# Optimization experiments

Hardware: AMD Instinct MI355X
Metric: run time of the kernel (lower is better)

## Reference

```python
import jax, jax.numpy as jnp
import numpy as np

H_STEP = 0.1
DT_MOMENTUM = 1.0
NUM_STEPS = 5
PAD_IDX = 0


def setup_inputs() -> dict:
    key = jax.random.key(0)
    k0, k1, k2, k3 = jax.random.split(key, 4)
    V, D, S, H, B = 32000, 512, 1024, 2048, 32
    table = jax.random.normal(k0, (V, D), jnp.float32) * 0.02
    log_masses = jnp.zeros((S,), jnp.float32)
    W1 = jax.random.normal(k1, (H, D), jnp.float32) * (1.0 / np.sqrt(D))
    b1 = jnp.zeros((H,), jnp.float32)
    W2 = jax.random.normal(k2, (1, H), jnp.float32) * (1.0 / np.sqrt(H))
    b2 = jnp.zeros((1,), jnp.float32)
    enc_input_ids = jax.random.randint(k3, (B, S), 0, V)
    return {"table": table, "log_masses": log_masses, "W1": W1, "b1": b1,
            "W2": W2, "b2": b2, "enc_input_ids": enc_input_ids}


def reference(table, log_masses, W1, b1, W2, b2, enc_input_ids):
    # padding mask derived as ids != pad_idx (code path with enc_padding_mask=None)
    mask = (enc_input_ids != PAD_IDX).astype(jnp.float32)[..., None]  # [B,S,1]
    # nn.Embedding(padding_idx=0): row 0 is zero
    row_mask = (jnp.arange(table.shape[0]) != PAD_IDX).astype(table.dtype)[:, None]
    tab = table * row_mask
    q0 = tab[enc_input_ids]                                            # [B,S,D]
    # replicate-pad one step in front -> finite-difference velocities
    prev = jnp.concatenate([q0[:, :1], q0[:, :-1]], axis=1)
    vel = (q0 - prev) / DT_MOMENTUM
    masses = jnp.exp(log_masses)[None, :, None]                        # [1,S,1]
    p0 = masses * vel * mask

    w2 = W2[0]  # [H]

    def force(q):
        # torch detaches q before the potential; grad through forces w.r.t. q is cut
        qs = jax.lax.stop_gradient(q)
        t = jnp.tanh(qs @ W1.T + b1)                                   # [B,S,H]
        # analytic grad of sum(mask * (tanh(qW1^T+b1) @ w2 + b2)) w.r.t. q
        g = ((1.0 - t * t) * w2) @ W1                                  # [B,S,D]
        return -(mask * g)

    def step(carry, _):
        q, p = carry
        f1 = force(q)
        p_half = p + 0.5 * H_STEP * f1
        q_delta = H_STEP * (p_half / masses) * mask
        q_next = q + q_delta
        f2 = force(q_next)
        p_next = (p_half + 0.5 * H_STEP * f2) * mask
        return (q_next, p_next), None

    (q, p), _ = jax.lax.scan(step, (q0, p0), None, length=NUM_STEPS)
    return (q, p)
```

## Files before the change

### kernel.cpp

```cpp
#include <hip/hip_runtime.h>

#define D_SZ 512
#define S_SZ 1024
#define H_SZ 2048
#define BS_SZ 32768
#define H_STEP 0.1f

typedef __attribute__((ext_vector_type(4))) float f32x4;
typedef __attribute__((ext_vector_type(8))) short s16x8;
typedef __attribute__((ext_vector_type(4))) unsigned short u16x4;
typedef unsigned short ushort_t;
typedef unsigned char u8;
typedef long long i64;

__device__ __forceinline__ ushort_t f2b(float f) {
    unsigned u = __float_as_uint(f);
    unsigned r = (u + 0x7FFFu + ((u >> 16) & 1u)) >> 16;
    return (ushort_t)r;
}
__device__ __forceinline__ float b2f(ushort_t b) {
    return __uint_as_float(((unsigned)b) << 16);
}

__device__ __forceinline__ void gload_lds16(const void* g, void* l) {
    __builtin_amdgcn_global_load_lds(
        (const __attribute__((address_space(1))) unsigned int*)g,
        (__attribute__((address_space(3))) unsigned int*)l, 16, 0, 0);
}

__global__ void prep_w1(const float* __restrict__ W1,
                        ushort_t* __restrict__ W1b) {
    int idx = blockIdx.x * 256 + threadIdx.x;
    W1b[idx] = f2b(W1[idx]);
}

__global__ void prep_w1t8(const float* __restrict__ W1, u8* __restrict__ W1f8) {
    __shared__ float t[64][65];
    int hb = blockIdx.x >> 3;
    int db = blockIdx.x & 7;
    int tr = threadIdx.x >> 2;
    int tc = threadIdx.x & 3;
    const float* src = W1 + (size_t)(hb * 64 + tr) * D_SZ + db * 64 + tc * 16;
    #pragma unroll
    for (int j = 0; j < 16; j += 4) {
        f32x4 v = *(const f32x4*)(src + j);
        t[tr][tc * 16 + j + 0] = v[0];
        t[tr][tc * 16 + j + 1] = v[1];
        t[tr][tc * 16 + j + 2] = v[2];
        t[tr][tc * 16 + j + 3] = v[3];
    }
    __syncthreads();
    u8* dst = W1f8 + (size_t)(db * 64 + tr) * H_SZ + hb * 64 + tc * 16;
    #pragma unroll
    for (int j = 0; j < 16; j += 4) {
        int r = 0;
        r = __builtin_amdgcn_cvt_pk_fp8_f32(t[tc * 16 + j + 0][tr] * 8.0f,
                                            t[tc * 16 + j + 1][tr] * 8.0f, r, false);
        r = __builtin_amdgcn_cvt_pk_fp8_f32(t[tc * 16 + j + 2][tr] * 8.0f,
                                            t[tc * 16 + j + 3][tr] * 8.0f, r, true);
        *(int*)(dst + j) = r;
    }
}

__global__ void prep_mass(const float* __restrict__ logm,
                          float* __restrict__ inv_mass,
                          float* __restrict__ mass) {
    int s = blockIdx.x * 256 + threadIdx.x;
    if (s < S_SZ) {
        float lm = logm[s];
        mass[s] = expf(lm);
        inv_mass[s] = expf(-lm);
    }
}

__global__ void embed_kernel(const float* __restrict__ table,
                             const int* __restrict__ ids,
                             const float* __restrict__ mass,
                             float* __restrict__ p,
                             ushort_t* __restrict__ qb) {
    int i = blockIdx.x;
    int t = threadIdx.x;
    int s = i & (S_SZ - 1);
    int id = ids[i];
    int idp = (s == 0) ? id : ids[i - 1];
    float mk = (id != 0) ? 1.f : 0.f;
    float ms = mass[s];
    int d0 = t * 4;

    f32x4 cur = {0.f, 0.f, 0.f, 0.f};
    f32x4 prv = {0.f, 0.f, 0.f, 0.f};
    if (id != 0)  cur = *(const f32x4*)(table + (size_t)id  * D_SZ + d0);
    if (idp != 0) prv = *(const f32x4*)(table + (size_t)idp * D_SZ + d0);

    size_t off = (size_t)i * D_SZ + d0;
    u16x4 cb;
    cb[0] = f2b(cur[0]); cb[1] = f2b(cur[1]); cb[2] = f2b(cur[2]); cb[3] = f2b(cur[3]);
    *(u16x4*)(qb + off) = cb;

    f32x4 pv;
    pv[0] = ms * (cur[0] - prv[0]) * mk;
    pv[1] = ms * (cur[1] - prv[1]) * mk;
    pv[2] = ms * (cur[2] - prv[2]) * mk;
    pv[3] = ms * (cur[3] - prv[3]) * mk;
    *(f32x4*)(p + off) = pv;
}

__global__ __launch_bounds__(1024, 4) void gemm_f1(
        const ushort_t* __restrict__ A,
        const ushort_t* __restrict__ B,
        const float* __restrict__ b1,
        const float* __restrict__ W2,
        u8* __restrict__ U) {
    constexpr int KLEN = 512;
    constexpr int NT = KLEN / 32;
    __shared__ __align__(16) ushort_t lA[3][256 * 32];
    __shared__ __align__(16) ushort_t lB[3][256 * 32];

    const int tid = threadIdx.x;
    const int lane = tid & 63, wid = tid >> 6;
    const int wg = wid >> 2, wn = wid & 3;
    const int lr = lane & 15, lk = lane >> 4;

    int wgid = ((int)blockIdx.x & 7) * 128 + ((int)blockIdx.x >> 3);
    int bxA = wgid & 7;
    int by  = wgid >> 3;
    const long a0 = (long)bxA * 256;
    const long b0 = (long)by * 256;

    const int r0  = tid >> 2;
    const int kc  = tid & 3;
    const int kcs = kc ^ ((r0 >> 1) & 3);
    const ushort_t* gA = A + (a0 + r0) * (long)KLEN + kcs * 8;
    const ushort_t* gB = B + (b0 + r0) * (long)KLEN + kcs * 8;

#define STAGE(t) { int _b = (t) % 3;                          \
    gload_lds16(gA + (long)(t) * 32, &lA[_b][tid * 8]);       \
    gload_lds16(gB + (long)(t) * 32, &lB[_b][tid * 8]); }

    f32x4 acc[4][4];
    #pragma unroll
    for (int m = 0; m < 4; ++m)
        #pragma unroll
        for (int n = 0; n < 4; ++n)
            acc[m][n] = (f32x4){0.f, 0.f, 0.f, 0.f};

    const int lks8 = (lk ^ ((lr >> 1) & 3)) * 8;
    const int roA = (wg * 64 + lr) * 32 + lks8;
    const int roB = (wn * 64 + lr) * 32 + lks8;

    STAGE(0);
    STAGE(1);

    for (int t = 0; t < NT; ++t) {
        const int buf = t % 3;
        const ushort_t* bA = &lA[buf][0];
        const ushort_t* bB = &lB[buf][0];
        if (t < NT - 1) asm volatile("s_waitcnt vmcnt(2)" ::: "memory");
        else           asm volatile("s_waitcnt vmcnt(0)" ::: "memory");
        __builtin_amdgcn_s_barrier();

        s16x8 av[4], bv[4];
        #pragma unroll
        for (int m = 0; m < 4; ++m) av[m] = *(const s16x8*)&bA[roA + m * 512];
        #pragma unroll
        for (int n = 0; n < 4; ++n) bv[n] = *(const s16x8*)&bB[roB + n * 512];
        asm volatile("s_waitcnt lgkmcnt(0)" ::: "memory");
        __builtin_amdgcn_sched_barrier(0);
        __builtin_amdgcn_s_setprio(1);
        #pragma unroll
        for (int m = 0; m < 4; ++m)
            #pragma unroll
            for (int n = 0; n < 4; ++n)
                acc[m][n] = __builtin_amdgcn_mfma_f32_16x16x32_bf16(av[m], bv[n], acc[m][n], 0, 0, 0);
        __builtin_amdgcn_s_setprio(0);
        __builtin_amdgcn_s_barrier();
        if (t + 2 < NT) STAGE(t + 2);
    }
#undef STAGE

    #pragma unroll
    for (int m = 0; m < 4; ++m) {
        long h0 = a0 + wg * 64 + m * 16 + lk * 4;
        f32x4 b1v = *(const f32x4*)(b1 + h0);
        f32x4 w2v = *(const f32x4*)(W2 + h0);
        #pragma unroll
        for (int n = 0; n < 4; ++n) {
            long i = b0 + wn * 64 + n * 16 + lr;
            float v[4];
            #pragma unroll
            for (int j = 0; j < 4; ++j) {
                float uu = acc[m][n][j] + b1v[j];
                float e = __expf(-2.0f * fabsf(uu));
                float rc = 1.0f / (1.0f + e);
                v[j] = 64.0f * e * rc * rc * w2v[j];
            }
            int pk = 0;
            pk = __builtin_amdgcn_cvt_pk_fp8_f32(v[0], v[1], pk, false);
            pk = __builtin_amdgcn_cvt_pk_fp8_f32(v[2], v[3], pk, true);
            *(int*)(U + i * H_SZ + h0) = pk;
        }
    }
}

__global__ __launch_bounds__(512, 2) void gemm_f2(
        const u8* __restrict__ W1f8,
        const u8* __restrict__ Uf8,
        const int* __restrict__ ids,
        const float* __restrict__ inv_mass,
        float* __restrict__ qf,
        float* __restrict__ p,
        ushort_t* __restrict__ qb,
        float coef, int do_q, int wq) {
    __shared__ __align__(16) u8 lA[2][256 * 64];
    __shared__ __align__(16) u8 lB[2][128 * 64];

    const int tid = threadIdx.x;
    const int lane = tid & 63, wid = tid >> 6;
    const int wd = wid >> 1, wi = wid & 1;
    const int lr = lane & 15, lk = lane >> 4;

    int wgid = ((int)blockIdx.x & 7) * 64 + ((int)blockIdx.x >> 3);
    const int  dh = wgid & 1;
    const long a0 = (long)dh * 256;
    const long b0 = (long)(wgid >> 1) * 128;

    const int r0  = tid >> 2;
    const int kc  = tid & 3;
    const int kcs = kc ^ ((r0 >> 1) & 3);
    const u8* gA = W1f8 + (a0 + r0) * (long)H_SZ + kcs * 16;
    const u8* gB = Uf8 + (b0 + r0) * (long)H_SZ + kcs * 16;

#define STG(t) { int _b = (t) & 1; \
    gload_lds16(gA + (long)(t) * 64,               &lA[_b][tid * 16]); \
    gload_lds16(gA + 128L * H_SZ + (long)(t) * 64, &lA[_b][(tid + 512) * 16]); \
    gload_lds16(gB + (long)(t) * 64,               &lB[_b][tid * 16]); }

    f32x4 acc[4][4];
    #pragma unroll
    for (int m = 0; m < 4; ++m)
        #pragma unroll
        for (int n = 0; n < 4; ++n)
            acc[m][n] = (f32x4){0.f, 0.f, 0.f, 0.f};

    const int key = (lr >> 1) & 3;

    STG(0);
    const int NT = H_SZ / 64;
    for (int t = 0; t < NT; ++t) {
        if (t + 1 < NT) {
            STG(t + 1);
            asm volatile("s_waitcnt vmcnt(3)" ::: "memory");
        } else {
            asm volatile("s_waitcnt vmcnt(0)" ::: "memory");
        }
        __builtin_amdgcn_s_barrier();

        const u8* bA = &lA[t & 1][0];
        const u8* bB = &lB[t & 1][0];
        #pragma unroll
        for (int x = 0; x < 2; ++x) {
            const int so = (((x * 2 + (lk >> 1)) ^ key) * 16) + (lk & 1) * 8;
            i64 a[4], b[4];
            #pragma unroll
            for (int m = 0; m < 4; ++m)
                a[m] = *(const i64*)&bA[(wd * 64 + m * 16 + lr) * 64 + so];
            #pragma unroll
            for (int n = 0; n < 4; ++n)
                b[n] = *(const i64*)&bB[(wi * 64 + n * 16 + lr) * 64 + so];
            asm volatile("s_waitcnt lgkmcnt(0)" ::: "memory");
            __builtin_amdgcn_sched_barrier(0);
            __builtin_amdgcn_s_setprio(1);
            #pragma unroll
            for (int m = 0; m < 4; ++m)
                #pragma unroll
                for (int n = 0; n < 4; ++n)
                    acc[m][n] = __builtin_amdgcn_mfma_f32_16x16x32_fp8_fp8(a[m], b[n], acc[m][n], 0, 0, 0);
            __builtin_amdgcn_s_setprio(0);
        }
        __builtin_amdgcn_s_barrier();
    }
#undef STG

    const float cs = coef * (1.0f / 128.0f);
    #pragma unroll
    for (int n = 0; n < 4; ++n) {
        long i = b0 + wi * 64 + n * 16 + lr;
        int id = ids[i];
        float cm = (id != 0) ? cs : 0.f;
        float hm = (id != 0) ? H_STEP : 0.f;
        float im = inv_mass[(int)(i & (S_SZ - 1))];
        #pragma unroll
        for (int m = 0; m < 4; ++m) {
            long d0 = a0 + wd * 64 + m * 16 + lk * 4;
            size_t off = (size_t)i * D_SZ + d0;
            f32x4 pv = *(const f32x4*)(p + off);
            #pragma unroll
            for (int j = 0; j < 4; ++j)
                pv[j] -= cm * acc[m][n][j];
            *(f32x4*)(p + off) = pv;
            if (do_q) {
                u16x4 qo = *(const u16x4*)(qb + off);
                f32x4 qv;
                u16x4 qn;
                #pragma unroll
                for (int j = 0; j < 4; ++j) {
                    qv[j] = b2f(qo[j]) + hm * pv[j] * im;
                    qn[j] = f2b(qv[j]);
                }
                *(u16x4*)(qb + off) = qn;
                if (wq) *(f32x4*)(qf + off) = qv;
            }
        }
    }
}

extern "C" void kernel_launch(void* const* d_in, const int* in_sizes, int n_in,
                              void* d_out, int out_size, void* d_ws, size_t ws_size,
                              hipStream_t stream) {
    const float* table = (const float*)d_in[0];
    const float* logm  = (const float*)d_in[1];
    const float* W1    = (const float*)d_in[2];
    const float* b1    = (const float*)d_in[3];
    const float* W2    = (const float*)d_in[4];
    const int*   ids   = (const int*)d_in[6];

    float* qf = (float*)d_out;
    float* p  = qf + (size_t)BS_SZ * D_SZ;

    char* ws = (char*)d_ws;
    size_t o = 0;
    ushort_t* qb  = (ushort_t*)(ws + o); o += (size_t)BS_SZ * D_SZ * 2;
    u8* Uf8       = (u8*)(ws + o);       o += (size_t)BS_SZ * H_SZ;
    ushort_t* W1b = (ushort_t*)(ws + o); o += (size_t)H_SZ * D_SZ * 2;
    u8* W1f8      = (u8*)(ws + o);       o += (size_t)D_SZ * H_SZ;
    float* inv_mass = (float*)(ws + o);  o += S_SZ * 4;
    float* mass     = (float*)(ws + o);  o += S_SZ * 4;

    prep_w1<<<(H_SZ * D_SZ) / 256, 256, 0, stream>>>(W1, W1b);
    prep_w1t8<<<256, 256, 0, stream>>>(W1, W1f8);
    prep_mass<<<(S_SZ + 255) / 256, 256, 0, stream>>>(logm, inv_mass, mass);
    embed_kernel<<<BS_SZ, 128, 0, stream>>>(table, ids, mass, p, qb);

    for (int j = 0; j < 6; ++j) {
        gemm_f1<<<1024, 1024, 0, stream>>>(W1b, qb, b1, W2, Uf8);
        float coef = (j == 0 || j == 5) ? 0.05f : 0.1f;
        gemm_f2<<<512, 512, 0, stream>>>(
            W1f8, Uf8, ids, inv_mass, qf, p, qb, coef, (j < 5) ? 1 : 0, (j == 4) ? 1 : 0);
    }
}
```

Measured before the change: 1.109 ms.

## Switch first force GEMM from bf16 to scaled fp8 MFMA

After: 1.093 ms. Within noise of the previous version (-1.5%).

```diff
diff --git a/kernel.cpp b/kernel.cpp
--- a/kernel.cpp
+++ b/kernel.cpp
@@ -28,10 +28,13 @@
         (__attribute__((address_space(3))) unsigned int*)l, 16, 0, 0);
 }
 
-__global__ void prep_w1(const float* __restrict__ W1,
-                        ushort_t* __restrict__ W1b) {
-    int idx = blockIdx.x * 256 + threadIdx.x;
-    W1b[idx] = f2b(W1[idx]);
+__global__ void prep_w1r8(const float* __restrict__ W1, u8* __restrict__ W1f8r) {
+    int idx4 = (blockIdx.x * 256 + threadIdx.x) * 4;
+    f32x4 v = *(const f32x4*)(W1 + idx4);
+    int r = 0;
+    r = __builtin_amdgcn_cvt_pk_fp8_f32(v[0] * 8.0f, v[1] * 8.0f, r, false);
+    r = __builtin_amdgcn_cvt_pk_fp8_f32(v[2] * 8.0f, v[3] * 8.0f, r, true);
+    *(int*)(W1f8r + idx4) = r;
 }
 
 __global__ void prep_w1t8(const float* __restrict__ W1, u8* __restrict__ W1f8) {
@@ -77,7 +80,8 @@
                              const int* __restrict__ ids,
                              const float* __restrict__ mass,
                              float* __restrict__ p,
-                             ushort_t* __restrict__ qb) {
+                             ushort_t* __restrict__ qb,
+                             u8* __restrict__ q8) {
     int i = blockIdx.x;
     int t = threadIdx.x;
     int s = i & (S_SZ - 1);
@@ -96,6 +100,10 @@
     u16x4 cb;
     cb[0] = f2b(cur[0]); cb[1] = f2b(cur[1]); cb[2] = f2b(cur[2]); cb[3] = f2b(cur[3]);
     *(u16x4*)(qb + off) = cb;
+    int pk8 = 0;
+    pk8 = __builtin_amdgcn_cvt_pk_fp8_f32(cur[0] * 32.f, cur[1] * 32.f, pk8, false);
+    pk8 = __builtin_amdgcn_cvt_pk_fp8_f32(cur[2] * 32.f, cur[3] * 32.f, pk8, true);
+    *(int*)(q8 + off) = pk8;
 
     f32x4 pv;
     pv[0] = ms * (cur[0] - prv[0]) * mk;
@@ -106,15 +114,15 @@
 }
 
 __global__ __launch_bounds__(1024, 4) void gemm_f1(
-        const ushort_t* __restrict__ A,
-        const ushort_t* __restrict__ B,
+        const u8* __restrict__ A,
+        const u8* __restrict__ B,
         const float* __restrict__ b1,
         const float* __restrict__ W2,
         u8* __restrict__ U) {
     constexpr int KLEN = 512;
-    constexpr int NT = KLEN / 32;
-    __shared__ __align__(16) ushort_t lA[3][256 * 32];
-    __shared__ __align__(16) ushort_t lB[3][256 * 32];
+    constexpr int NT = KLEN / 64;
+    __shared__ __align__(16) u8 lA[3][256 * 64];
+    __shared__ __align__(16) u8 lB[3][256 * 64];
 
     const int tid = threadIdx.x;
     const int lane = tid & 63, wid = tid >> 6;
@@ -130,12 +138,12 @@
     const int r0  = tid >> 2;
     const int kc  = tid & 3;
     const int kcs = kc ^ ((r0 >> 1) & 3);
-    const ushort_t* gA = A + (a0 + r0) * (long)KLEN + kcs * 8;
-    const ushort_t* gB = B + (b0 + r0) * (long)KLEN + kcs * 8;
-
-#define STAGE(t) { int _b = (t) % 3;                          \
-    gload_lds16(gA + (long)(t) * 32, &lA[_b][tid * 8]);       \
-    gload_lds16(gB + (long)(t) * 32, &lB[_b][tid * 8]); }
+    const u8* gA = A + (a0 + r0) * (long)KLEN + kcs * 16;
+    const u8* gB = B + (b0 + r0) * (long)KLEN + kcs * 16;
+
+#define STAGE(t) { int _b = (t) % 3;                           \
+    gload_lds16(gA + (long)(t) * 64, &lA[_b][tid * 16]);       \
+    gload_lds16(gB + (long)(t) * 64, &lB[_b][tid * 16]); }
 
     f32x4 acc[4][4];
     #pragma unroll
@@ -144,35 +152,39 @@
         for (int n = 0; n < 4; ++n)
             acc[m][n] = (f32x4){0.f, 0.f, 0.f, 0.f};
 
-    const int lks8 = (lk ^ ((lr >> 1) & 3)) * 8;
-    const int roA = (wg * 64 + lr) * 32 + lks8;
-    const int roB = (wn * 64 + lr) * 32 + lks8;
+    const int key = (lr >> 1) & 3;
 
     STAGE(0);
     STAGE(1);
 
     for (int t = 0; t < NT; ++t) {
         const int buf = t % 3;
-        const ushort_t* bA = &lA[buf][0];
-        const ushort_t* bB = &lB[buf][0];
+        const u8* bA = &lA[buf][0];
+        const u8* bB = &lB[buf][0];
         if (t < NT - 1) asm volatile("s_waitcnt vmcnt(2)" ::: "memory");
         else           asm volatile("s_waitcnt vmcnt(0)" ::: "memory");
         __builtin_amdgcn_s_barrier();
 
-        s16x8 av[4], bv[4];
-        #pragma unroll
-        for (int m = 0; m < 4; ++m) av[m] = *(const s16x8*)&bA[roA + m * 512];
-        #pragma unroll
-        for (int n = 0; n < 4; ++n) bv[n] = *(const s16x8*)&bB[roB + n * 512];
-        asm volatile("s_waitcnt lgkmcnt(0)" ::: "memory");
-        __builtin_amdgcn_sched_barrier(0);
-        __builtin_amdgcn_s_setprio(1);
-        #pragma unroll
-        for (int m = 0; m < 4; ++m)
+        #pragma unroll
+        for (int x = 0; x < 2; ++x) {
+            const int so = (((x * 2 + (lk >> 1)) ^ key) * 16) + (lk & 1) * 8;
+            i64 a[4], b[4];
+            #pragma unroll
+            for (int m = 0; m < 4; ++m)
+                a[m] = *(const i64*)&bA[(wg * 64 + m * 16 + lr) * 64 + so];
             #pragma unroll
             for (int n = 0; n < 4; ++n)
-                acc[m][n] = __builtin_amdgcn_mfma_f32_16x16x32_bf16(av[m], bv[n], acc[m][n], 0, 0, 0);
-        __builtin_amdgcn_s_setprio(0);
+                b[n] = *(const i64*)&bB[(wn * 64 + n * 16 + lr) * 64 + so];
+            asm volatile("s_waitcnt lgkmcnt(0)" ::: "memory");
+            __builtin_amdgcn_sched_barrier(0);
+            __builtin_amdgcn_s_setprio(1);
+            #pragma unroll
+            for (int m = 0; m < 4; ++m)
+                #pragma unroll
+                for (int n = 0; n < 4; ++n)
+                    acc[m][n] = __builtin_amdgcn_mfma_f32_16x16x32_fp8_fp8(a[m], b[n], acc[m][n], 0, 0, 0);
+            __builtin_amdgcn_s_setprio(0);
+        }
         __builtin_amdgcn_s_barrier();
         if (t + 2 < NT) STAGE(t + 2);
     }
@@ -189,7 +201,7 @@
             float v[4];
             #pragma unroll
             for (int j = 0; j < 4; ++j) {
-                float uu = acc[m][n][j] + b1v[j];
+                float uu = acc[m][n][j] * 0.00390625f + b1v[j];
                 float e = __expf(-2.0f * fabsf(uu));
                 float rc = 1.0f / (1.0f + e);
                 v[j] = 64.0f * e * rc * rc * w2v[j];
@@ -210,6 +222,7 @@
         float* __restrict__ qf,
         float* __restrict__ p,
         ushort_t* __restrict__ qb,
+        u8* __restrict__ q8,
         float coef, int do_q, int wq) {
     __shared__ __align__(16) u8 lA[2][256 * 64];
     __shared__ __align__(16) u8 lB[2][128 * 64];
@@ -308,6 +321,10 @@
                     qn[j] = f2b(qv[j]);
                 }
                 *(u16x4*)(qb + off) = qn;
+                int pk8 = 0;
+                pk8 = __builtin_amdgcn_cvt_pk_fp8_f32(qv[0] * 32.f, qv[1] * 32.f, pk8, false);
+                pk8 = __builtin_amdgcn_cvt_pk_fp8_f32(qv[2] * 32.f, qv[3] * 32.f, pk8, true);
+                *(int*)(q8 + off) = pk8;
                 if (wq) *(f32x4*)(qf + off) = qv;
             }
         }
@@ -330,21 +347,22 @@
     char* ws = (char*)d_ws;
     size_t o = 0;
     ushort_t* qb  = (ushort_t*)(ws + o); o += (size_t)BS_SZ * D_SZ * 2;
+    u8* q8        = (u8*)(ws + o);       o += (size_t)BS_SZ * D_SZ;
     u8* Uf8       = (u8*)(ws + o);       o += (size_t)BS_SZ * H_SZ;
-    ushort_t* W1b = (ushort_t*)(ws + o); o += (size_t)H_SZ * D_SZ * 2;
+    u8* W1f8r     = (u8*)(ws + o);       o += (size_t)H_SZ * D_SZ;
     u8* W1f8      = (u8*)(ws + o);       o += (size_t)D_SZ * H_SZ;
     float* inv_mass = (float*)(ws + o);  o += S_SZ * 4;
     float* mass     = (float*)(ws + o);  o += S_SZ * 4;
 
-    prep_w1<<<(H_SZ * D_SZ) / 256, 256, 0, stream>>>(W1, W1b);
+    prep_w1r8<<<(H_SZ * D_SZ) / 1024, 256, 0, stream>>>(W1, W1f8r);
     prep_w1t8<<<256, 256, 0, stream>>>(W1, W1f8);
     prep_mass<<<(S_SZ + 255) / 256, 256, 0, stream>>>(logm, inv_mass, mass);
-    embed_kernel<<<BS_SZ, 128, 0, stream>>>(table, ids, mass, p, qb);
+    embed_kernel<<<BS_SZ, 128, 0, stream>>>(table, ids, mass, p, qb, q8);
 
     for (int j = 0; j < 6; ++j) {
-        gemm_f1<<<1024, 1024, 0, stream>>>(W1b, qb, b1, W2, Uf8);
+        gemm_f1<<<1024, 1024, 0, stream>>>(W1f8r, q8, b1, W2, Uf8);
         float coef = (j == 0 || j == 5) ? 0.05f : 0.1f;
         gemm_f2<<<512, 512, 0, stream>>>(
-            W1f8, Uf8, ids, inv_mass, qf, p, qb, coef, (j < 5) ? 1 : 0, (j == 4) ? 1 : 0);
-    }
-}
+            W1f8, Uf8, ids, inv_mass, qf, p, qb, q8, coef, (j < 5) ? 1 : 0, (j == 4) ? 1 : 0);
+    }
+}
```
